# Performance work log

Measured on AMD Instinct MI355X. Metric: run time of the kernel, lower is better.

## Reference

```python
import jax, jax.numpy as jnp
import numpy as np

N, M, E = 400000, 100000, 3200000
C_FEAT = 61            # per-point feature channels
D_IN = 64              # 3 (rel xyz) + C_FEAT
D0, D1, D2 = 64, 128, 256  # mlp = [64, 128, 256]
EPS = 1e-5


def setup_inputs() -> dict:
    key = jax.random.key(0)
    ks = jax.random.split(key, 16)
    inp = {}
    inp['point_bxyz'] = jax.random.uniform(ks[0], (N, 4), dtype=jnp.float32) * 50.0
    inp['point_feat'] = jax.random.normal(ks[1], (N, C_FEAT), dtype=jnp.float32)
    inp['sample_idx'] = jax.random.randint(ks[2], (M,), 0, N)
    inp['e_point'] = jax.random.randint(ks[3], (E,), 0, N)
    inp['e_new'] = jnp.sort(jax.random.randint(ks[4], (E,), 0, M))
    # PointConv: Linear(D_IN -> D0)
    inp['W0'] = jax.random.normal(ks[5], (D_IN, D0), dtype=jnp.float32) / np.sqrt(D_IN)
    inp['b0'] = jnp.zeros((D0,), dtype=jnp.float32)
    # mlp_convs[0]: Linear(D0 -> D1) + BN
    inp['W1'] = jax.random.normal(ks[6], (D0, D1), dtype=jnp.float32) / np.sqrt(D0)
    inp['b1'] = jnp.zeros((D1,), dtype=jnp.float32)
    inp['g1'] = jnp.ones((D1,), dtype=jnp.float32)
    inp['beta1'] = jnp.zeros((D1,), dtype=jnp.float32)
    # mlp_convs[1]: Linear(D1 -> D2) + BN
    inp['W2'] = jax.random.normal(ks[7], (D1, D2), dtype=jnp.float32) / np.sqrt(D1)
    inp['b2'] = jnp.zeros((D2,), dtype=jnp.float32)
    inp['g2'] = jnp.ones((D2,), dtype=jnp.float32)
    inp['beta2'] = jnp.zeros((D2,), dtype=jnp.float32)
    return inp


def _bn_relu(x, g, b):
    # BatchNorm1d in training mode: batch stats, biased variance
    mu = x.mean(axis=0)
    var = x.var(axis=0)
    return jax.nn.relu((x - mu) * jax.lax.rsqrt(var + EPS) * g + b)


def reference(point_bxyz, point_feat, sample_idx, e_point, e_new,
              W0, b0, W1, b1, g1, beta1, W2, b2, g2, beta2):
    num_new = sample_idx.shape[0]
    new_bxyz = point_bxyz[sample_idx]                      # [M, 4]
    # PointConv: per-edge relative position encoding + feature gather
    rel = point_bxyz[e_point, 1:4] - new_bxyz[e_new, 1:4]  # [E, 3]
    edge_in = jnp.concatenate([rel, point_feat[e_point]], axis=-1)  # [E, D_IN]
    h = jax.nn.relu(edge_in @ W0 + b0)                     # [E, D0]
    # per-neighborhood max aggregation (scatter-max), empty segments -> 0
    agg = jax.ops.segment_max(h, e_new, num_segments=num_new)
    agg = jnp.where(jnp.isneginf(agg), 0.0, agg)           # [M, D0]
    # trailing Linear + BN + ReLU stack
    x = _bn_relu(agg @ W1 + b1, g1, beta1)                 # [M, D1]
    x = _bn_relu(x @ W2 + b2, g2, beta2)                   # [M, D2]
    return new_bxyz, x
```

## Files before the change

kernel.cpp:

```cpp
#include <hip/hip_runtime.h>

#define EPS 1e-5f
#define ECHUNK 64
#define PF 8

typedef _Float16 half8 __attribute__((ext_vector_type(8)));
typedef _Float16 half4v __attribute__((ext_vector_type(4)));
typedef float float4v __attribute__((ext_vector_type(4)));

__global__ void gather_kernel(const float4* __restrict__ bxyz, const int* __restrict__ sidx,
                              float4* __restrict__ out, int M) {
    int i = blockIdx.x * blockDim.x + threadIdx.x;
    if (i < M) out[i] = bxyz[sidx[i]];
}

__global__ void prep_kernel(const float* __restrict__ W0, const float* __restrict__ W1,
                            const float* __restrict__ W2, _Float16* __restrict__ W0t,
                            _Float16* __restrict__ W1t, _Float16* __restrict__ W2t) {
    int i = blockIdx.x * blockDim.x + threadIdx.x;
    if (i < 4096) {
        int k = i >> 6, n = i & 63;
        W0t[(size_t)n * 64 + k] = (_Float16)W0[i];
    } else if (i < 12288) {
        int j = i - 4096; int k = j >> 7, n = j & 127;
        W1t[(size_t)n * 64 + k] = (_Float16)W1[j];
    } else if (i < 45056) {
        int j = i - 12288; int k = j >> 8, n = j & 255;
        W2t[(size_t)n * 128 + k] = (_Float16)W2[j];
    }
}

__global__ __launch_bounds__(256, 4) void point_kernel(
    const float* __restrict__ feat, const float4* __restrict__ bxyz4,
    const _Float16* __restrict__ W0t, const float* __restrict__ b0,
    _Float16* __restrict__ GDh, int N) {
    __shared__ _Float16 As[128 * 72];
    int t = threadIdx.x;
    int row0 = blockIdx.x * 128;
    if (t < 128) {
        int r = min(row0 + t, N - 1);
        float4 P = bxyz4[r];
        As[t * 72 + 0] = (_Float16)P.y;
        As[t * 72 + 1] = (_Float16)P.z;
        As[t * 72 + 2] = (_Float16)P.w;
    }
    const float* fbase = feat + (size_t)row0 * 61;
    int avail = (int)min((size_t)7808, (size_t)(N - row0) * 61);
#pragma unroll
    for (int j = 0; j < 8; ++j) {
        int base = (t + j * 256) * 4;
        if (base < avail) {
            float4 v = *(const float4*)&fbase[base];
            float fv[4] = {v.x, v.y, v.z, v.w};
#pragma unroll
            for (int u = 0; u < 4; ++u) {
                int flat = base + u;
                int r = flat / 61;
                int k = flat - r * 61;
                As[r * 72 + 3 + k] = (_Float16)fv[u];
            }
        }
    }
    __syncthreads();
    int w = t >> 6, lane = t & 63, quad = lane >> 4, l16 = lane & 15;
    int mwave = w * 32;
    float4v acc[2][4] = {};
#pragma unroll
    for (int kc = 0; kc < 2; ++kc) {
        int koff = kc * 32 + quad * 8;
        half8 af[2], bf[4];
#pragma unroll
        for (int mt = 0; mt < 2; ++mt)
            af[mt] = *(const half8*)&As[(mwave + mt * 16 + l16) * 72 + koff];
#pragma unroll
        for (int nt = 0; nt < 4; ++nt)
            bf[nt] = *(const half8*)&W0t[(size_t)(nt * 16 + l16) * 64 + koff];
#pragma unroll
        for (int mt = 0; mt < 2; ++mt)
#pragma unroll
            for (int nt = 0; nt < 4; ++nt)
                acc[mt][nt] = __builtin_amdgcn_mfma_f32_16x16x32_f16(af[mt], bf[nt], acc[mt][nt], 0, 0, 0);
    }
    float b0v[4];
#pragma unroll
    for (int nt = 0; nt < 4; ++nt) b0v[nt] = b0[nt * 16 + l16];
    __syncthreads();
#pragma unroll
    for (int mt = 0; mt < 2; ++mt)
#pragma unroll
        for (int i = 0; i < 4; ++i) {
            int rloc = mwave + mt * 16 + quad * 4 + i;
#pragma unroll
            for (int nt = 0; nt < 4; ++nt)
                As[rloc * 72 + nt * 16 + l16] = (_Float16)(acc[mt][nt][i] + b0v[nt]);
        }
    __syncthreads();
#pragma unroll
    for (int j = 0; j < 4; ++j) {
        int i8 = t + j * 256;
        int r = i8 >> 3, c8 = i8 & 7;
        if (row0 + r < N)
            *(half8*)&GDh[(size_t)(row0 + r) * 64 + c8 * 8] = *(const half8*)&As[r * 72 + c8 * 8];
    }
}

__global__ __launch_bounds__(256, 4) void edge_kernel(
    const float4* __restrict__ nbxyz4,
    const int* __restrict__ e_point, const int* __restrict__ e_new,
    const _Float16* __restrict__ GDh, const float* __restrict__ W0,
    float* __restrict__ agg, int E) {
    int lane = threadIdx.x & 63;
    int gwave = blockIdx.x * 4 + (threadIdx.x >> 6);
    int base = gwave * ECHUNK;
    if (base >= E) return;
    int n = min(ECHUNK, E - base);
    int idx = min(base + lane, E - 1);
    int ep = e_point[idx];
    int en = e_new[idx];
    float wx = W0[lane], wy = W0[64 + lane], wz = W0[128 + lane];
    float runmax = 0.f;
    int curseg = -1;
    float S = 0.f;
    for (int g0 = 0; g0 < n; g0 += PF) {
        _Float16 gu[PF];
#pragma unroll
        for (int j = 0; j < PF; ++j) {
            int p = __builtin_amdgcn_readlane(ep, g0 + j);
            gu[j] = GDh[(size_t)p * 64 + lane];
        }
#pragma unroll
        for (int j = 0; j < PF; ++j) {
            if (g0 + j >= n) break;
            int s = __builtin_amdgcn_readlane(en, g0 + j);
            if (s != curseg) {
                if (curseg >= 0)
                    atomicMax((int*)&agg[(size_t)curseg * 64 + lane], __float_as_int(runmax));
                curseg = s;
                runmax = 0.f;
                float4 Q = nbxyz4[s];
                S = fmaf(Q.y, wx, fmaf(Q.z, wy, Q.w * wz));
            }
            float h = (float)gu[j] - S;
            runmax = fmaxf(runmax, h);
        }
    }
    if (curseg >= 0)
        atomicMax((int*)&agg[(size_t)curseg * 64 + lane], __float_as_int(runmax));
}

__global__ __launch_bounds__(256, 2) void gemm1_kernel(
    const float* __restrict__ agg, const _Float16* __restrict__ W1t,
    _Float16* __restrict__ y1h, float* __restrict__ p1sum, float* __restrict__ p1sq, int M) {
    __shared__ _Float16 As[128 * 72];
    __shared__ float red[4096];
    int t = threadIdx.x;
    int row0 = blockIdx.x * 128;
#pragma unroll
    for (int j = 0; j < 8; ++j) {
        int i4 = t + j * 256;
        int r = i4 >> 4, k4 = i4 & 15;
        float4 v = make_float4(0.f, 0.f, 0.f, 0.f);
        if (row0 + r < M) v = ((const float4*)agg)[(size_t)(row0 + r) * 16 + k4];
        half4v h;
        h[0] = (_Float16)v.x; h[1] = (_Float16)v.y; h[2] = (_Float16)v.z; h[3] = (_Float16)v.w;
        *(half4v*)&As[r * 72 + k4 * 4] = h;
    }
    __syncthreads();
    int w = t >> 6, lane = t & 63, quad = lane >> 4, l16 = lane & 15;
    int mwave = w * 32;
    float4v acc[2][8] = {};
#pragma unroll
    for (int kc = 0; kc < 2; ++kc) {
        int koff = kc * 32 + quad * 8;
        half8 af[2], bf[8];
#pragma unroll
        for (int mt = 0; mt < 2; ++mt)
            af[mt] = *(const half8*)&As[(mwave + mt * 16 + l16) * 72 + koff];
#pragma unroll
        for (int nt = 0; nt < 8; ++nt)
            bf[nt] = *(const half8*)&W1t[(size_t)(nt * 16 + l16) * 64 + koff];
#pragma unroll
        for (int mt = 0; mt < 2; ++mt)
#pragma unroll
            for (int nt = 0; nt < 8; ++nt)
                acc[mt][nt] = __builtin_amdgcn_mfma_f32_16x16x32_f16(af[mt], bf[nt], acc[mt][nt], 0, 0, 0);
    }
    float s[8] = {}, q[8] = {};
#pragma unroll
    for (int mt = 0; mt < 2; ++mt)
#pragma unroll
        for (int i = 0; i < 4; ++i)
#pragma unroll
            for (int nt = 0; nt < 8; ++nt) {
                float a = acc[mt][nt][i];
                s[nt] += a; q[nt] += a * a;
            }
    int slot = w * 4 + quad;
#pragma unroll
    for (int nt = 0; nt < 8; ++nt) {
        int c = nt * 16 + l16;
        red[c * 16 + slot] = s[nt];
        red[2048 + c * 16 + slot] = q[nt];
    }
    __syncthreads();
    if (t < 128) {
        float ss = 0.f, qq = 0.f;
#pragma unroll
        for (int i = 0; i < 16; ++i) { ss += red[t * 16 + i]; qq += red[2048 + t * 16 + i]; }
        p1sum[(size_t)blockIdx.x * 128 + t] = ss;
        p1sq[(size_t)blockIdx.x * 128 + t] = qq;
    }
#pragma unroll
    for (int half = 0; half < 2; ++half) {
#pragma unroll
        for (int mt = 0; mt < 2; ++mt)
#pragma unroll
            for (int i = 0; i < 4; ++i) {
                int rloc = mwave + mt * 16 + quad * 4 + i;
#pragma unroll
                for (int nt = 0; nt < 4; ++nt)
                    As[rloc * 72 + nt * 16 + l16] = (_Float16)acc[mt][half * 4 + nt][i];
            }
        __syncthreads();
#pragma unroll
        for (int j = 0; j < 4; ++j) {
            int i8 = t + j * 256;
            int r = i8 >> 3, c8 = i8 & 7;
            if (row0 + r < M)
                *(half8*)&y1h[(size_t)(row0 + r) * 128 + half * 64 + c8 * 8] =
                    *(const half8*)&As[r * 72 + c8 * 8];
        }
        __syncthreads();
    }
}

__global__ void stats_kernel(const float* __restrict__ psum, const float* __restrict__ psq,
                             const float* __restrict__ g, const float* __restrict__ beta,
                             float* __restrict__ scale, float* __restrict__ shift,
                             int nblk, int ncols, float invM) {
    __shared__ float ss[256], qq[256];
    int c = blockIdx.x;
    int t = threadIdx.x;
    float s = 0.f, q = 0.f;
    for (int b = t; b < nblk; b += 256) {
        s += psum[(size_t)b * ncols + c];
        q += psq[(size_t)b * ncols + c];
    }
    ss[t] = s; qq[t] = q;
    __syncthreads();
    for (int off = 128; off > 0; off >>= 1) {
        if (t < off) { ss[t] += ss[t + off]; qq[t] += qq[t + off]; }
        __syncthreads();
    }
    if (t == 0) {
        float mean = ss[0] * invM;
        float var = qq[0] * invM - mean * mean;
        float sc = g[c] * rsqrtf(var + EPS);
        scale[c] = sc;
        shift[c] = beta[c] - mean * sc;
    }
}

__global__ __launch_bounds__(256, 2) void gemm2_kernel(
    const _Float16* __restrict__ y1h, const _Float16* __restrict__ W2t,
    const float* __restrict__ scale1, const float* __restrict__ shift1,
    float* __restrict__ yout, float* __restrict__ p2sum, float* __restrict__ p2sq,
    int M, int nbn) {
    __shared__ _Float16 As[128 * 136];
    __shared__ _Float16 Bs[128 * 136];
    int t = threadIdx.x;
    int bm = blockIdx.x / nbn;
    int bn = blockIdx.x % nbn;
    int row0 = bm * 128;
#pragma unroll
    for (int j = 0; j < 8; ++j) {
        int i8 = t + j * 256;
        int r = i8 >> 4, k8 = i8 & 15;
        half8 hv = {};
        if (row0 + r < M) {
            half8 y = *(const half8*)&y1h[(size_t)(row0 + r) * 128 + k8 * 8];
            float4 sca = ((const float4*)scale1)[k8 * 2];
            float4 scb = ((const float4*)scale1)[k8 * 2 + 1];
            float4 sha = ((const float4*)shift1)[k8 * 2];
            float4 shb = ((const float4*)shift1)[k8 * 2 + 1];
            float sc[8] = {sca.x, sca.y, sca.z, sca.w, scb.x, scb.y, scb.z, scb.w};
            float sh[8] = {sha.x, sha.y, sha.z, sha.w, shb.x, shb.y, shb.z, shb.w};
#pragma unroll
            for (int u = 0; u < 8; ++u)
                hv[u] = (_Float16)fmaxf(0.f, fmaf((float)y[u], sc[u], sh[u]));
        }
        *(half8*)&As[r * 136 + k8 * 8] = hv;
    }
    int n0 = bn * 128;
#pragma unroll
    for (int j = 0; j < 8; ++j) {
        int i8 = t + j * 256;
        int nn = i8 >> 4, k8 = i8 & 15;
        *(half8*)&Bs[nn * 136 + k8 * 8] = *(const half8*)&W2t[(size_t)(n0 + nn) * 128 + k8 * 8];
    }
    __syncthreads();
    int w = t >> 6, lane = t & 63;
    int quad = lane >> 4, l16 = lane & 15;
    int mwave = (w >> 1) * 64, nwave = (w & 1) * 64;
    float4v acc[4][4] = {};
#pragma unroll
    for (int kc = 0; kc < 4; ++kc) {
        int koff = kc * 32 + quad * 8;
        half8 af[4], bf[4];
#pragma unroll
        for (int mt = 0; mt < 4; ++mt)
            af[mt] = *(const half8*)&As[(mwave + mt * 16 + l16) * 136 + koff];
#pragma unroll
        for (int nt = 0; nt < 4; ++nt)
            bf[nt] = *(const half8*)&Bs[(nwave + nt * 16 + l16) * 136 + koff];
#pragma unroll
        for (int mt = 0; mt < 4; ++mt)
#pragma unroll
            for (int nt = 0; nt < 4; ++nt)
                acc[mt][nt] = __builtin_amdgcn_mfma_f32_16x16x32_f16(af[mt], bf[nt], acc[mt][nt], 0, 0, 0);
    }
    float s[4] = {}, q[4] = {};
    int colbase = n0 + nwave + l16;
#pragma unroll
    for (int mt = 0; mt < 4; ++mt) {
#pragma unroll
        for (int i = 0; i < 4; ++i) {
            int row = row0 + mwave + mt * 16 + quad * 4 + i;
            if (row < M) {
#pragma unroll
                for (int nt = 0; nt < 4; ++nt)
                    yout[(size_t)row * 256 + colbase + nt * 16] = acc[mt][nt][i];
            }
#pragma unroll
            for (int nt = 0; nt < 4; ++nt) {
                float a = acc[mt][nt][i];
                s[nt] += a; q[nt] += a * a;
            }
        }
    }
    __syncthreads();
    float* red = (float*)As;
    int slot = (w >> 1) * 4 + quad;
#pragma unroll
    for (int nt = 0; nt < 4; ++nt) {
        int c = (w & 1) * 64 + nt * 16 + l16;
        red[c * 8 + slot] = s[nt];
        red[1024 + c * 8 + slot] = q[nt];
    }
    __syncthreads();
    if (t < 128) {
        float ss = 0.f, qq = 0.f;
#pragma unroll
        for (int i = 0; i < 8; ++i) { ss += red[t * 8 + i]; qq += red[1024 + t * 8 + i]; }
        p2sum[(size_t)bm * 256 + n0 + t] = ss;
        p2sq[(size_t)bm * 256 + n0 + t] = qq;
    }
}

__global__ void apply2_kernel(float4* __restrict__ x, const float* __restrict__ scale2,
                              const float* __restrict__ shift2, int n4) {
    int i = blockIdx.x * blockDim.x + threadIdx.x;
    if (i >= n4) return;
    int c4 = i & 63;
    float4 v = x[i];
    float4 sc = ((const float4*)scale2)[c4];
    float4 sh = ((const float4*)shift2)[c4];
    v.x = fmaxf(0.f, fmaf(v.x, sc.x, sh.x));
    v.y = fmaxf(0.f, fmaf(v.y, sc.y, sh.y));
    v.z = fmaxf(0.f, fmaf(v.z, sc.z, sh.z));
    v.w = fmaxf(0.f, fmaf(v.w, sc.w, sh.w));
    x[i] = v;
}

extern "C" void kernel_launch(void* const* d_in, const int* in_sizes, int n_in,
                              void* d_out, int out_size, void* d_ws, size_t ws_size,
                              hipStream_t stream) {
    const float* bxyz  = (const float*)d_in[0];
    const float* feat  = (const float*)d_in[1];
    const int*   sidx  = (const int*)d_in[2];
    const int*   e_point = (const int*)d_in[3];
    const int*   e_new = (const int*)d_in[4];
    const float* W0    = (const float*)d_in[5];
    const float* b0    = (const float*)d_in[6];
    const float* W1    = (const float*)d_in[7];
    const float* g1    = (const float*)d_in[9];
    const float* beta1 = (const float*)d_in[10];
    const float* W2    = (const float*)d_in[11];
    const float* g2    = (const float*)d_in[13];
    const float* beta2 = (const float*)d_in[14];
    int N = in_sizes[0] / 4;
    int M = in_sizes[2];
    int E = in_sizes[3];

    float* out0 = (float*)d_out;
    float* out1 = (float*)d_out + (size_t)M * 4;

    float* ws = (float*)d_ws;
    size_t o = 0;
    float* agg = ws + o; o += (size_t)M * 64;
    _Float16* y1h = (_Float16*)(ws + o); o += (size_t)M * 64;
    _Float16* GDh = (_Float16*)(ws + o); o += (size_t)N * 32;
    _Float16* W0t = (_Float16*)(ws + o); o += 2048;
    _Float16* W1t = (_Float16*)(ws + o); o += 4096;
    _Float16* W2t = (_Float16*)(ws + o); o += 16384;
    int nblk1 = (M + 127) / 128;
    int nblk2m = (M + 127) / 128;
    int nbn = 2;
    float* p1sum = ws + o; o += (size_t)nblk1 * 128;
    float* p1sq  = ws + o; o += (size_t)nblk1 * 128;
    float* p2sum = ws + o; o += (size_t)nblk2m * 256;
    float* p2sq  = ws + o; o += (size_t)nblk2m * 256;
    float* scale1 = ws + o; o += 128;
    float* shift1 = ws + o; o += 128;
    float* scale2 = ws + o; o += 256;
    float* shift2 = ws + o; o += 256;

    hipMemsetAsync(agg, 0, (size_t)M * 64 * sizeof(float), stream);
    gather_kernel<<<(M + 255) / 256, 256, 0, stream>>>((const float4*)bxyz, sidx, (float4*)out0, M);
    prep_kernel<<<176, 256, 0, stream>>>(W0, W1, W2, W0t, W1t, W2t);
    point_kernel<<<(N + 127) / 128, 256, 0, stream>>>(feat, (const float4*)bxyz, W0t, b0, GDh, N);
    int nwaves = (E + ECHUNK - 1) / ECHUNK;
    edge_kernel<<<(nwaves + 3) / 4, 256, 0, stream>>>((const float4*)out0, e_point, e_new,
                                                      GDh, W0, agg, E);
    gemm1_kernel<<<nblk1, 256, 0, stream>>>(agg, W1t, y1h, p1sum, p1sq, M);
    stats_kernel<<<128, 256, 0, stream>>>(p1sum, p1sq, g1, beta1, scale1, shift1, nblk1, 128, 1.f / M);
    gemm2_kernel<<<nblk2m * nbn, 256, 0, stream>>>(y1h, W2t, scale1, shift1, out1, p2sum, p2sq, M, nbn);
    stats_kernel<<<256, 256, 0, stream>>>(p2sum, p2sq, g2, beta2, scale2, shift2, nblk2m, 256, 1.f / M);
    apply2_kernel<<<((M * 64) + 255) / 256, 256, 0, stream>>>((float4*)out1, scale2, shift2, M * 64);
}
```

Baseline: 402.9 us.

## Precompute segment boundaries via ballot and defer xyz offset to segment flush

The edge kernel now finds segment boundaries once per wave with a shuffle-up and ballot into a scalar mask, and fully unrolls the full-chunk path. Because the xyz term is constant within a segment, max(g - S) equals max(g) - S, so it keeps a running fp16 max of raw gathered features and subtracts S and applies ReLU only when a segment is flushed. This removes per-edge subtraction and float conversion and turns the per-edge boundary compare into a scalar bit test. Occupancy is raised to 8 waves per SIMD. The fp16 running max adds a little rounding relative to the fp32 path, and the higher occupancy target may constrain registers.

```diff
diff --git a/kernel.cpp b/kernel.cpp
--- a/kernel.cpp
+++ b/kernel.cpp
@@ -104,48 +104,80 @@
     }
 }
 
-__global__ __launch_bounds__(256, 4) void edge_kernel(
+__global__ __launch_bounds__(256, 8) void edge_kernel(
     const float4* __restrict__ nbxyz4,
     const int* __restrict__ e_point, const int* __restrict__ e_new,
     const _Float16* __restrict__ GDh, const float* __restrict__ W0,
     float* __restrict__ agg, int E) {
     int lane = threadIdx.x & 63;
     int gwave = blockIdx.x * 4 + (threadIdx.x >> 6);
-    int base = gwave * ECHUNK;
+    int base = __builtin_amdgcn_readfirstlane(gwave * ECHUNK);
     if (base >= E) return;
     int n = min(ECHUNK, E - base);
     int idx = min(base + lane, E - 1);
     int ep = e_point[idx];
     int en = e_new[idx];
     float wx = W0[lane], wy = W0[64 + lane], wz = W0[128 + lane];
-    float runmax = 0.f;
-    int curseg = -1;
-    float S = 0.f;
-    for (int g0 = 0; g0 < n; g0 += PF) {
-        _Float16 gu[PF];
-#pragma unroll
-        for (int j = 0; j < PF; ++j) {
-            int p = __builtin_amdgcn_readlane(ep, g0 + j);
-            gu[j] = GDh[(size_t)p * 64 + lane];
-        }
-#pragma unroll
-        for (int j = 0; j < PF; ++j) {
-            if (g0 + j >= n) break;
-            int s = __builtin_amdgcn_readlane(en, g0 + j);
-            if (s != curseg) {
-                if (curseg >= 0)
-                    atomicMax((int*)&agg[(size_t)curseg * 64 + lane], __float_as_int(runmax));
-                curseg = s;
-                runmax = 0.f;
-                float4 Q = nbxyz4[s];
-                S = fmaf(Q.y, wx, fmaf(Q.z, wy, Q.w * wz));
-            }
-            float h = (float)gu[j] - S;
-            runmax = fmaxf(runmax, h);
-        }
-    }
-    if (curseg >= 0)
-        atomicMax((int*)&agg[(size_t)curseg * 64 + lane], __float_as_int(runmax));
+
+    int prev = __shfl_up(en, 1);
+    unsigned long long bm = __ballot(lane == 0 || en != prev);
+    unsigned blo = __builtin_amdgcn_readfirstlane((unsigned)bm);
+    unsigned bhi = __builtin_amdgcn_readfirstlane((unsigned)(bm >> 32));
+    unsigned long long bmask = ((unsigned long long)bhi << 32) | blo;
+
+    int curseg = __builtin_amdgcn_readlane(en, 0);
+    _Float16 m16 = (_Float16)(-65504.f);
+
+#define FLUSH_SEG()  do {                                                         \
+        float4 Q = nbxyz4[curseg];                                                \
+        float S = fmaf(Q.y, wx, fmaf(Q.z, wy, Q.w * wz));                         \
+        float v = fmaxf(0.f, (float)m16 - S);                                     \
+        atomicMax((int*)&agg[(size_t)curseg * 64 + lane], __float_as_int(v));     \
+    } while (0)
+
+    if (n == ECHUNK) {
+#pragma unroll
+        for (int g0 = 0; g0 < ECHUNK; g0 += PF) {
+            _Float16 gu[PF];
+#pragma unroll
+            for (int j = 0; j < PF; ++j) {
+                int p = __builtin_amdgcn_readlane(ep, g0 + j);
+                gu[j] = GDh[(size_t)p * 64 + lane];
+            }
+#pragma unroll
+            for (int j = 0; j < PF; ++j) {
+                int e = g0 + j;
+                if (e > 0 && ((bmask >> e) & 1)) {
+                    FLUSH_SEG();
+                    curseg = __builtin_amdgcn_readlane(en, e);
+                    m16 = (_Float16)(-65504.f);
+                }
+                m16 = __builtin_fmaxf16(m16, gu[j]);
+            }
+        }
+    } else {
+        for (int g0 = 0; g0 < n; g0 += PF) {
+            _Float16 gu[PF];
+#pragma unroll
+            for (int j = 0; j < PF; ++j) {
+                int p = __builtin_amdgcn_readlane(ep, g0 + j);
+                gu[j] = GDh[(size_t)p * 64 + lane];
+            }
+#pragma unroll
+            for (int j = 0; j < PF; ++j) {
+                int e = g0 + j;
+                if (e >= n) break;
+                if (e > 0 && ((bmask >> e) & 1)) {
+                    FLUSH_SEG();
+                    curseg = __builtin_amdgcn_readlane(en, e);
+                    m16 = (_Float16)(-65504.f);
+                }
+                m16 = __builtin_fmaxf16(m16, gu[j]);
+            }
+        }
+    }
+    FLUSH_SEG();
+#undef FLUSH_SEG
 }
 
 __global__ __launch_bounds__(256, 2) void gemm1_kernel(
```

New measurement: 391.2 us. -2.9%, faster.

## Process two edges per wave-step with packed fp16 max in edge kernel

Applied to the files above, without the earlier changes.

The full-chunk path of the edge kernel now has each half-wave load a 32-bit pair of fp16 channels for a different edge, so one wave handles two edges per step. The running max is kept as packed half2 with v_pk_max_f16. Segment boundaries come from a ballot bitmask, and the halves are combined with a shuffle before the position term is subtracted and the atomic max is issued. Occupancy bounds are raised to 8 blocks per CU. The aim is fewer load instructions and less per-edge ALU and branch work. The cost is more complex flush logic, and the position term plus ReLU is now applied after the max rather than per edge, which is algebraically equivalent.

```diff
diff --git a/kernel.cpp b/kernel.cpp
--- a/kernel.cpp
+++ b/kernel.cpp
@@ -2,11 +2,16 @@
 
 #define EPS 1e-5f
 #define ECHUNK 64
-#define PF 8
 
 typedef _Float16 half8 __attribute__((ext_vector_type(8)));
 typedef _Float16 half4v __attribute__((ext_vector_type(4)));
 typedef float float4v __attribute__((ext_vector_type(4)));
+
+static __device__ __forceinline__ unsigned pkmax16(unsigned a, unsigned b) {
+    unsigned d;
+    asm("v_pk_max_f16 %0, %1, %2" : "=v"(d) : "v"(a), "v"(b));
+    return d;
+}
 
 __global__ void gather_kernel(const float4* __restrict__ bxyz, const int* __restrict__ sidx,
                               float4* __restrict__ out, int M) {
@@ -104,34 +109,88 @@
     }
 }
 
-__global__ __launch_bounds__(256, 4) void edge_kernel(
+__global__ __launch_bounds__(256, 8) void edge_kernel(
     const float4* __restrict__ nbxyz4,
     const int* __restrict__ e_point, const int* __restrict__ e_new,
     const _Float16* __restrict__ GDh, const float* __restrict__ W0,
     float* __restrict__ agg, int E) {
     int lane = threadIdx.x & 63;
     int gwave = blockIdx.x * 4 + (threadIdx.x >> 6);
-    int base = gwave * ECHUNK;
+    int base = __builtin_amdgcn_readfirstlane(gwave * ECHUNK);
     if (base >= E) return;
     int n = min(ECHUNK, E - base);
-    int idx = min(base + lane, E - 1);
-    int ep = e_point[idx];
-    int en = e_new[idx];
-    float wx = W0[lane], wy = W0[64 + lane], wz = W0[128 + lane];
-    float runmax = 0.f;
-    int curseg = -1;
-    float S = 0.f;
-    for (int g0 = 0; g0 < n; g0 += PF) {
-        _Float16 gu[PF];
-#pragma unroll
-        for (int j = 0; j < PF; ++j) {
-            int p = __builtin_amdgcn_readlane(ep, g0 + j);
-            gu[j] = GDh[(size_t)p * 64 + lane];
-        }
-#pragma unroll
-        for (int j = 0; j < PF; ++j) {
-            if (g0 + j >= n) break;
-            int s = __builtin_amdgcn_readlane(en, g0 + j);
+
+    if (n == ECHUNK) {
+        bool hi = lane >= 32;
+        int c0 = lane & 31;
+        int ch = c0 * 2 + (hi ? 1 : 0);
+        float wx = W0[ch], wy = W0[64 + ch], wz = W0[128 + ch];
+        const unsigned NEGP = 0xFBFFFBFFu;
+
+        int ep = e_point[base + lane];
+        int en = e_new[base + lane];
+
+        int prev = __shfl_up(en, 1);
+        unsigned long long bm = __ballot(lane == 0 || en != prev);
+        unsigned blo = __builtin_amdgcn_readfirstlane((unsigned)bm);
+        unsigned bhi = __builtin_amdgcn_readfirstlane((unsigned)(bm >> 32));
+        unsigned long long bmask = (((unsigned long long)bhi << 32) | blo) & ~1ull;
+
+        int curseg = __builtin_amdgcn_readlane(en, 0);
+        unsigned amax = NEGP;
+        int laneoff = c0 * 4;
+        int permbase = hi ? 4 : 0;
+
+#define FLUSH_SEG()  do {                                                          \
+        unsigned other_ = (unsigned)__shfl_xor((int)amax, 32);                     \
+        unsigned comb_ = pkmax16(amax, other_);                                    \
+        unsigned bits_ = hi ? (comb_ >> 16) : (comb_ & 0xffffu);                   \
+        _Float16 hm_ = __builtin_bit_cast(_Float16, (unsigned short)bits_);        \
+        float4 Q_ = nbxyz4[curseg];                                                \
+        float S_ = fmaf(Q_.y, wx, fmaf(Q_.z, wy, Q_.w * wz));                      \
+        float v_ = fmaxf(0.f, (float)hm_ - S_);                                    \
+        atomicMax((int*)&agg[(size_t)curseg * 64 + ch], __float_as_int(v_));       \
+    } while (0)
+
+#pragma unroll
+        for (int grp = 0; grp < 2; ++grp) {
+            unsigned gu[16];
+#pragma unroll
+            for (int j = 0; j < 16; ++j) {
+                int p = __builtin_amdgcn_ds_bpermute(permbase + (grp * 16 + j) * 8, ep);
+                unsigned off = ((unsigned)p << 7) + laneoff;
+                gu[j] = *(const unsigned*)((const char*)GDh + off);
+            }
+#pragma unroll
+            for (int j = 0; j < 16; ++j) {
+                int e0 = (grp * 16 + j) * 2;
+                if ((bmask >> e0) & 1) {
+                    FLUSH_SEG();
+                    curseg = __builtin_amdgcn_readlane(en, e0);
+                    amax = NEGP;
+                }
+                if ((bmask >> (e0 + 1)) & 1) {
+                    amax = pkmax16(amax, hi ? NEGP : gu[j]);
+                    FLUSH_SEG();
+                    curseg = __builtin_amdgcn_readlane(en, e0 + 1);
+                    amax = hi ? gu[j] : NEGP;
+                } else {
+                    amax = pkmax16(amax, gu[j]);
+                }
+            }
+        }
+        FLUSH_SEG();
+#undef FLUSH_SEG
+    } else {
+        float wx = W0[lane], wy = W0[64 + lane], wz = W0[128 + lane];
+        int idx = min(base + lane, E - 1);
+        int ep = e_point[idx];
+        int en = e_new[idx];
+        int curseg = -1;
+        float runmax = 0.f, S = 0.f;
+        for (int e = 0; e < n; ++e) {
+            int p = __builtin_amdgcn_readlane(ep, e);
+            int s = __builtin_amdgcn_readlane(en, e);
             if (s != curseg) {
                 if (curseg >= 0)
                     atomicMax((int*)&agg[(size_t)curseg * 64 + lane], __float_as_int(runmax));
@@ -140,12 +199,12 @@
                 float4 Q = nbxyz4[s];
                 S = fmaf(Q.y, wx, fmaf(Q.z, wy, Q.w * wz));
             }
-            float h = (float)gu[j] - S;
+            float h = (float)GDh[(size_t)p * 64 + lane] - S;
             runmax = fmaxf(runmax, h);
         }
-    }
-    if (curseg >= 0)
-        atomicMax((int*)&agg[(size_t)curseg * 64 + lane], __float_as_int(runmax));
+        if (curseg >= 0)
+            atomicMax((int*)&agg[(size_t)curseg * 64 + lane], __float_as_int(runmax));
+    }
 }
 
 __global__ __launch_bounds__(256, 2) void gemm1_kernel(
```

After: 389.0 us. -3.4%, faster.
